# Kernel optimization log

Hardware: AMD Instinct MI355X
Metric: run time of the kernel (lower is better)

The kernel has to match this reference:

```python
import jax, jax.numpy as jnp
import numpy as np


def setup_inputs() -> dict:
    key = jax.random.key(0)
    k1, k2, k3 = jax.random.split(key, 3)
    B, H, I, O, Dp1 = 4, 2048, 1024, 1024, 4  # degree=3 -> degree+1=4
    x = jax.random.normal(k1, (B, H, I, Dp1), dtype=jnp.float32)
    weight = 0.1 * jax.random.normal(k2, (O, Dp1), dtype=jnp.float32)
    weighted_sum = 0.1 * jax.random.normal(k3, (O, I), dtype=jnp.float32)
    return {"x": x, "weight": weight, "weighted_sum": weighted_sum}


def reference(x, weight, weighted_sum):
    # Original: weights[o,i,d] = weighted_sum[o,i] * weight[o,d];
    #           out[b,h,o] = sum_{i,d} x[b,h,i,d] * weights[o,i,d]
    # Fused 3-operand einsum avoids materializing the (O, I, D+1) intermediate.
    return jnp.einsum('bhid,oi,od->bho', x, weighted_sum, weight)
```

## Files before the change

### kernel.cpp

```cpp
#include <hip/hip_runtime.h>

typedef unsigned short u16;
typedef u16 u16x4 __attribute__((ext_vector_type(4)));
typedef float f32x4 __attribute__((ext_vector_type(4)));
typedef __bf16 bf16x8 __attribute__((ext_vector_type(8)));

#define M_DIM 8192
#define N_DIM 1024
#define K_DIM 4096

__device__ __forceinline__ u16 f2bf(float f) {
  unsigned u = __float_as_uint(f);
  u += 0x7FFFu + ((u >> 16) & 1u);
  return (u16)(u >> 16);
}

__global__ __launch_bounds__(256) void k_cvt(const float* __restrict__ x,
                                             u16* __restrict__ y) {
  long i = ((long)blockIdx.x * 256 + threadIdx.x) * 4;
  f32x4 a = *(const f32x4*)(x + i);
  u16x4 r;
  r[0] = f2bf(a[0]); r[1] = f2bf(a[1]); r[2] = f2bf(a[2]); r[3] = f2bf(a[3]);
  *(u16x4*)(y + i) = r;
}

__global__ __launch_bounds__(256) void k_w2(const float* __restrict__ w,
                                            const float* __restrict__ ws,
                                            u16* __restrict__ w2) {
  int idx = blockIdx.x * 256 + threadIdx.x;
  int o = idx >> 10;
  float s = ws[idx];
  f32x4 wv = *(const f32x4*)(w + o * 4);
  u16x4 r;
  r[0] = f2bf(s * wv[0]); r[1] = f2bf(s * wv[1]);
  r[2] = f2bf(s * wv[2]); r[3] = f2bf(s * wv[3]);
  *(u16x4*)(w2 + (size_t)idx * 4) = r;
}

typedef __attribute__((address_space(1))) const void gvoid_t;
typedef __attribute__((address_space(3))) void lvoid_t;
__device__ __forceinline__ void gll16(const void* g, void* l) {
  __builtin_amdgcn_global_load_lds((gvoid_t*)g, (lvoid_t*)l, 16, 0, 0);
}

__global__ __launch_bounds__(512) void k_gemm(const u16* __restrict__ A,
                                              const u16* __restrict__ Bt,
                                              float* __restrict__ C) {
  __shared__ u16 sA[128 * 64];
  __shared__ u16 sB[128 * 64];

  const int t    = threadIdx.x;
  const int lane = t & 63;
  const int wid  = t >> 6;
  const int m0   = blockIdx.y * 128;
  const int n0   = blockIdx.x * 128;

  const int s0 = t, s1 = t + 512;
  const int r0 = s0 >> 3, c0 = (s0 & 7) ^ (r0 & 7);
  const int r1 = s1 >> 3, c1 = (s1 & 7) ^ (r1 & 7);
  const u16* gA0 = A  + (size_t)(m0 + r0) * K_DIM + c0 * 8;
  const u16* gA1 = A  + (size_t)(m0 + r1) * K_DIM + c1 * 8;
  const u16* gB0 = Bt + (size_t)(n0 + r0) * K_DIM + c0 * 8;
  const u16* gB1 = Bt + (size_t)(n0 + r1) * K_DIM + c1 * 8;
  u16* lA0 = sA + s0 * 8;  u16* lA1 = sA + s1 * 8;
  u16* lB0 = sB + s0 * 8;  u16* lB1 = sB + s1 * 8;

  const int wm = (wid >> 1) * 32;
  const int wn = (wid & 1) * 64;
  const int fr = lane & 15;
  const int lc = lane >> 4;

  f32x4 acc[2][4];
#pragma unroll
  for (int i = 0; i < 2; i++)
#pragma unroll
    for (int j = 0; j < 4; j++) acc[i][j] = (f32x4){0.f, 0.f, 0.f, 0.f};

  for (int k0 = 0; k0 < K_DIM; k0 += 64) {
    gll16(gA0, lA0); gll16(gA1, lA1);
    gll16(gB0, lB0); gll16(gB1, lB1);
    gA0 += 64; gA1 += 64; gB0 += 64; gB1 += 64;
    __syncthreads();

#pragma unroll
    for (int ks = 0; ks < 2; ks++) {
      bf16x8 af[2], bf[4];
#pragma unroll
      for (int mi = 0; mi < 2; mi++) {
        int r  = wm + mi * 16 + fr;
        int pc = (ks * 4 + lc) ^ (r & 7);
        af[mi] = *(const bf16x8*)(sA + r * 64 + pc * 8);
      }
#pragma unroll
      for (int ni = 0; ni < 4; ni++) {
        int r  = wn + ni * 16 + fr;
        int pc = (ks * 4 + lc) ^ (r & 7);
        bf[ni] = *(const bf16x8*)(sB + r * 64 + pc * 8);
      }
#pragma unroll
      for (int mi = 0; mi < 2; mi++)
#pragma unroll
        for (int ni = 0; ni < 4; ni++)
          acc[mi][ni] = __builtin_amdgcn_mfma_f32_16x16x32_bf16(
              af[mi], bf[ni], acc[mi][ni], 0, 0, 0);
    }
    __syncthreads();
  }

  const int cr = (lane >> 4) * 4;
  const int cc = lane & 15;
#pragma unroll
  for (int mi = 0; mi < 2; mi++)
#pragma unroll
    for (int ni = 0; ni < 4; ni++) {
      float* cp = C + (size_t)(m0 + wm + mi * 16 + cr) * N_DIM +
                  (n0 + wn + ni * 16 + cc);
#pragma unroll
      for (int r = 0; r < 4; r++) cp[(size_t)r * N_DIM] = acc[mi][ni][r];
    }
}

extern "C" void kernel_launch(void* const* d_in, const int* in_sizes, int n_in,
                              void* d_out, int out_size, void* d_ws, size_t ws_size,
                              hipStream_t stream) {
  const float* x  = (const float*)d_in[0];
  const float* w  = (const float*)d_in[1];
  const float* ws = (const float*)d_in[2];
  float* out = (float*)d_out;

  u16* xbf = (u16*)d_ws;
  u16* w2  = xbf + (size_t)M_DIM * K_DIM;

  k_cvt<<<32768, 256, 0, stream>>>(x, xbf);
  k_w2<<<4096, 256, 0, stream>>>(w, ws, w2);

  dim3 grid(N_DIM / 128, M_DIM / 128);
  k_gemm<<<grid, 512, 0, stream>>>(xbf, w2, out);
}
```

Measured before the change: 278.9 us.

## Fuse fp32-to-bf16 conversion of x into GEMM with double-buffered 256x128 tiles

Removes the separate conversion kernel. The GEMM now loads fp32 x directly into registers, converts it to bf16 and stores it into double-buffered LDS, while B is still loaded through global_load_lds. The tile grows to 256x128 with BK=32, uses a software pipeline with explicit waitcnt, barriers and setprio, and remaps blocks so each XCD gets contiguous M rows. This avoids writing and rereading a 64MB bf16 copy of x, but it reads twice as many A bytes inside the GEMM and depends on fragile hand-written vmcnt counts.

```diff
diff --git a/kernel.cpp b/kernel.cpp
--- a/kernel.cpp
+++ b/kernel.cpp
@@ -8,20 +8,14 @@
 #define M_DIM 8192
 #define N_DIM 1024
 #define K_DIM 4096
+#define BM 256
+#define BN 128
+#define BK 32
 
 __device__ __forceinline__ u16 f2bf(float f) {
   unsigned u = __float_as_uint(f);
   u += 0x7FFFu + ((u >> 16) & 1u);
   return (u16)(u >> 16);
-}
-
-__global__ __launch_bounds__(256) void k_cvt(const float* __restrict__ x,
-                                             u16* __restrict__ y) {
-  long i = ((long)blockIdx.x * 256 + threadIdx.x) * 4;
-  f32x4 a = *(const f32x4*)(x + i);
-  u16x4 r;
-  r[0] = f2bf(a[0]); r[1] = f2bf(a[1]); r[2] = f2bf(a[2]); r[3] = f2bf(a[3]);
-  *(u16x4*)(y + i) = r;
 }
 
 __global__ __launch_bounds__(256) void k_w2(const float* __restrict__ w,
@@ -43,74 +37,144 @@
   __builtin_amdgcn_global_load_lds((gvoid_t*)g, (lvoid_t*)l, 16, 0, 0);
 }
 
-__global__ __launch_bounds__(512) void k_gemm(const u16* __restrict__ A,
+__global__ __launch_bounds__(512) void k_gemm(const float* __restrict__ A,
                                               const u16* __restrict__ Bt,
                                               float* __restrict__ C) {
-  __shared__ u16 sA[128 * 64];
-  __shared__ u16 sB[128 * 64];
+  __shared__ u16 lds[24576];
+  u16* const sA0 = lds;
+  u16* const sA1 = lds + 8192;
+  u16* const sB0 = lds + 16384;
+  u16* const sB1 = lds + 20480;
 
   const int t    = threadIdx.x;
   const int lane = t & 63;
   const int wid  = t >> 6;
-  const int m0   = blockIdx.y * 128;
-  const int n0   = blockIdx.x * 128;
 
-  const int s0 = t, s1 = t + 512;
-  const int r0 = s0 >> 3, c0 = (s0 & 7) ^ (r0 & 7);
-  const int r1 = s1 >> 3, c1 = (s1 & 7) ^ (r1 & 7);
-  const u16* gA0 = A  + (size_t)(m0 + r0) * K_DIM + c0 * 8;
-  const u16* gA1 = A  + (size_t)(m0 + r1) * K_DIM + c1 * 8;
-  const u16* gB0 = Bt + (size_t)(n0 + r0) * K_DIM + c0 * 8;
-  const u16* gB1 = Bt + (size_t)(n0 + r1) * K_DIM + c1 * 8;
-  u16* lA0 = sA + s0 * 8;  u16* lA1 = sA + s1 * 8;
-  u16* lB0 = sB + s0 * 8;  u16* lB1 = sB + s1 * 8;
+  const int L   = blockIdx.x;
+  const int xcd = L & 7;
+  const int jb  = L >> 3;
+  const int m0  = (xcd * 4 + (jb >> 3)) * BM;
+  const int n0  = (jb & 7) * BN;
 
-  const int wm = (wid >> 1) * 32;
+  const int cg0 = (t & 3) ^ ((t >> 3) & 3);
+  const int r0  = t >> 2;
+  const float* gA0 = A + (size_t)(m0 + r0) * K_DIM + cg0 * 8;
+  const float* gA1 = A + (size_t)(m0 + 128 + r0) * K_DIM + cg0 * 8;
+  const int lAd0 = t * 8;
+  const int lAd1 = 4096 + t * 8;
+  const u16* gB = Bt + (size_t)(n0 + r0) * K_DIM + cg0 * 8;
+  const int dBo = t * 8;
+
+  const int wm = (wid >> 1) * 64;
   const int wn = (wid & 1) * 64;
   const int fr = lane & 15;
   const int lc = lane >> 4;
 
-  f32x4 acc[2][4];
+  int aoff[4], boff[4];
 #pragma unroll
-  for (int i = 0; i < 2; i++)
+  for (int i = 0; i < 4; i++) {
+    int ra = wm + i * 16 + fr;
+    aoff[i] = ra * 32 + ((lc ^ ((ra >> 1) & 3)) << 3);
+    int rb = wn + i * 16 + fr;
+    boff[i] = rb * 32 + ((lc ^ ((rb >> 1) & 3)) << 3);
+  }
+
+  f32x4 acc[4][4];
+#pragma unroll
+  for (int i = 0; i < 4; i++)
 #pragma unroll
     for (int j = 0; j < 4; j++) acc[i][j] = (f32x4){0.f, 0.f, 0.f, 0.f};
 
-  for (int k0 = 0; k0 < K_DIM; k0 += 64) {
-    gll16(gA0, lA0); gll16(gA1, lA1);
-    gll16(gB0, lB0); gll16(gB1, lB1);
-    gA0 += 64; gA1 += 64; gB0 += 64; gB1 += 64;
-    __syncthreads();
+  f32x4 xa, xb, xc, xd;
+  f32x4 ya, yb, yc, yd;
 
-#pragma unroll
-    for (int ks = 0; ks < 2; ks++) {
-      bf16x8 af[2], bf[4];
-#pragma unroll
-      for (int mi = 0; mi < 2; mi++) {
-        int r  = wm + mi * 16 + fr;
-        int pc = (ks * 4 + lc) ^ (r & 7);
-        af[mi] = *(const bf16x8*)(sA + r * 64 + pc * 8);
-      }
-#pragma unroll
-      for (int ni = 0; ni < 4; ni++) {
-        int r  = wn + ni * 16 + fr;
-        int pc = (ks * 4 + lc) ^ (r & 7);
-        bf[ni] = *(const bf16x8*)(sB + r * 64 + pc * 8);
-      }
-#pragma unroll
-      for (int mi = 0; mi < 2; mi++)
-#pragma unroll
-        for (int ni = 0; ni < 4; ni++)
-          acc[mi][ni] = __builtin_amdgcn_mfma_f32_16x16x32_bf16(
-              af[mi], bf[ni], acc[mi][ni], 0, 0, 0);
-    }
-    __syncthreads();
+#define STORESET(bufA, pa, pb, pc, pd)                          \
+  do {                                                          \
+    bf16x8 v0, v1;                                              \
+    v0[0] = (__bf16)pa[0]; v0[1] = (__bf16)pa[1];               \
+    v0[2] = (__bf16)pa[2]; v0[3] = (__bf16)pa[3];               \
+    v0[4] = (__bf16)pb[0]; v0[5] = (__bf16)pb[1];               \
+    v0[6] = (__bf16)pb[2]; v0[7] = (__bf16)pb[3];               \
+    v1[0] = (__bf16)pc[0]; v1[1] = (__bf16)pc[1];               \
+    v1[2] = (__bf16)pc[2]; v1[3] = (__bf16)pc[3];               \
+    v1[4] = (__bf16)pd[0]; v1[5] = (__bf16)pd[1];               \
+    v1[6] = (__bf16)pd[2]; v1[7] = (__bf16)pd[3];               \
+    *(bf16x8*)((bufA) + lAd0) = v0;                             \
+    *(bf16x8*)((bufA) + lAd1) = v1;                             \
+  } while (0)
+
+#define TILE(pAc, pBc, pAn, pBs, la, lb, lcr, ld, sa, sb, sc, sd, kb, ka)   \
+  do {                                                                      \
+    bf16x8 af0, af1, bq0, bq1, bq2, bq3;                                    \
+    af0 = *(const bf16x8*)((pAc) + aoff[0]);                                \
+    af1 = *(const bf16x8*)((pAc) + aoff[1]);                                \
+    bq0 = *(const bf16x8*)((pBc) + boff[0]);                                \
+    bq1 = *(const bf16x8*)((pBc) + boff[1]);                                \
+    bq2 = *(const bf16x8*)((pBc) + boff[2]);                                \
+    bq3 = *(const bf16x8*)((pBc) + boff[3]);                                \
+    gll16(gB + (kb), (pBs) + dBo);                                          \
+    la  = *(const f32x4*)(gA0 + (ka));                                      \
+    lb  = *(const f32x4*)(gA0 + (ka) + 4);                                  \
+    lcr = *(const f32x4*)(gA1 + (ka));                                      \
+    ld  = *(const f32x4*)(gA1 + (ka) + 4);                                  \
+    asm volatile("s_waitcnt vmcnt(5)" ::: "memory");                        \
+    STORESET(pAn, sa, sb, sc, sd);                                          \
+    __builtin_amdgcn_s_barrier();                                           \
+    asm volatile("s_waitcnt lgkmcnt(0)" ::: "memory");                      \
+    __builtin_amdgcn_s_setprio(1);                                          \
+    _Pragma("unroll")                                                       \
+    for (int n_ = 0; n_ < 4; n_++) {                                        \
+      bf16x8 bz = n_ == 0 ? bq0 : n_ == 1 ? bq1 : n_ == 2 ? bq2 : bq3;      \
+      acc[0][n_] = __builtin_amdgcn_mfma_f32_16x16x32_bf16(af0, bz,         \
+                                                           acc[0][n_], 0, 0, 0); \
+      acc[1][n_] = __builtin_amdgcn_mfma_f32_16x16x32_bf16(af1, bz,         \
+                                                           acc[1][n_], 0, 0, 0); \
+    }                                                                       \
+    __builtin_amdgcn_s_setprio(0);                                          \
+    __builtin_amdgcn_s_barrier();                                           \
+    af0 = *(const bf16x8*)((pAc) + aoff[2]);                                \
+    af1 = *(const bf16x8*)((pAc) + aoff[3]);                                \
+    asm volatile("s_waitcnt vmcnt(4)" ::: "memory");                        \
+    __builtin_amdgcn_s_barrier();                                           \
+    asm volatile("s_waitcnt lgkmcnt(0)" ::: "memory");                      \
+    __builtin_amdgcn_s_setprio(1);                                          \
+    _Pragma("unroll")                                                       \
+    for (int n_ = 0; n_ < 4; n_++) {                                        \
+      bf16x8 bz = n_ == 0 ? bq0 : n_ == 1 ? bq1 : n_ == 2 ? bq2 : bq3;      \
+      acc[2][n_] = __builtin_amdgcn_mfma_f32_16x16x32_bf16(af0, bz,         \
+                                                           acc[2][n_], 0, 0, 0); \
+      acc[3][n_] = __builtin_amdgcn_mfma_f32_16x16x32_bf16(af1, bz,         \
+                                                           acc[3][n_], 0, 0, 0); \
+    }                                                                       \
+    __builtin_amdgcn_s_setprio(0);                                          \
+    __builtin_amdgcn_s_barrier();                                           \
+  } while (0)
+
+  xa = *(const f32x4*)(gA0);      xb = *(const f32x4*)(gA0 + 4);
+  xc = *(const f32x4*)(gA1);      xd = *(const f32x4*)(gA1 + 4);
+  asm volatile("s_waitcnt vmcnt(0)" ::: "memory");
+  STORESET(sA0, xa, xb, xc, xd);
+  gll16(gB, sB0 + dBo);
+  ya = *(const f32x4*)(gA0 + 32); yb = *(const f32x4*)(gA0 + 36);
+  yc = *(const f32x4*)(gA1 + 32); yd = *(const f32x4*)(gA1 + 36);
+  asm volatile("s_waitcnt vmcnt(4) lgkmcnt(0)" ::: "memory");
+  __builtin_amdgcn_s_barrier();
+
+  for (int it = 0; it < 64; ++it) {
+    const int t0 = 2 * it;
+    TILE(sA0, sB0, sA1, sB1, xa, xb, xc, xd, ya, yb, yc, yd,
+         ((t0 + 1) & 127) * 32, ((t0 + 2) & 127) * 32);
+    TILE(sA1, sB1, sA0, sB0, ya, yb, yc, yd, xa, xb, xc, xd,
+         ((t0 + 2) & 127) * 32, ((t0 + 3) & 127) * 32);
   }
+
+#undef TILE
+#undef STORESET
 
   const int cr = (lane >> 4) * 4;
   const int cc = lane & 15;
 #pragma unroll
-  for (int mi = 0; mi < 2; mi++)
+  for (int mi = 0; mi < 4; mi++)
 #pragma unroll
     for (int ni = 0; ni < 4; ni++) {
       float* cp = C + (size_t)(m0 + wm + mi * 16 + cr) * N_DIM +
@@ -128,12 +192,8 @@
   const float* ws = (const float*)d_in[2];
   float* out = (float*)d_out;
 
-  u16* xbf = (u16*)d_ws;
-  u16* w2  = xbf + (size_t)M_DIM * K_DIM;
+  u16* w2 = (u16*)d_ws;
 
-  k_cvt<<<32768, 256, 0, stream>>>(x, xbf);
   k_w2<<<4096, 256, 0, stream>>>(w, ws, w2);
-
-  dim3 grid(N_DIM / 128, M_DIM / 128);
-  k_gemm<<<grid, 512, 0, stream>>>(xbf, w2, out);
+  k_gemm<<<256, 512, 0, stream>>>(x, w2, out);
 }
```

Result: slower. 327.7 us (+17.5%).
